# Kernel tuning notes

Measured on AMD Instinct MI355X. Metric: run time of the kernel, lower is better.

Reference implementation:

```python
import jax, jax.numpy as jnp
from jax import lax
import numpy as np

B, N, E, F = 32, 256, 8, 16
NEIGH = 31            # neighbourhood_size
K1 = NEIGH + 1        # subgraph size = neigh_size + 1


def setup_inputs() -> dict:
    rng = np.random.default_rng(0)
    # Connected symmetric adjacency: backbone chain + random extra pairs (no self loops).
    A = np.zeros((B, N, N), np.float32)
    i = np.arange(N - 1)
    A[:, i, i + 1] = 1.0
    A[:, i + 1, i] = 1.0
    for b in range(B):
        pairs = rng.integers(0, N, size=(N, 2))
        pairs = pairs[pairs[:, 0] != pairs[:, 1]]
        A[b, pairs[:, 0], pairs[:, 1]] = 1.0
        A[b, pairs[:, 1], pairs[:, 0]] = 1.0
    A[:, np.arange(N), np.arange(N)] = 0.0
    key = jax.random.key(0)
    k1, k2 = jax.random.split(key)
    edges = jax.random.normal(k1, (B, N, N, E), dtype=jnp.float32)
    feats = jax.random.normal(k2, (B, N, F), dtype=jnp.float32)
    return {"adj_batch": jnp.asarray(A), "edges_batch": edges, "features_batch": feats}


def _bfs(adj_bool, start):
    """Ordered BFS from `start`, collecting K1 vertices (matches get_neighbours:
    FIFO queue, neighbours enqueued in ascending index order, dedup vs seen)."""
    n = adj_bool.shape[0]
    queue = jnp.zeros((n + 1,), jnp.int32).at[0].set(start)  # slot n is a dummy sink
    seen = jnp.zeros((n,), bool).at[start].set(True)
    processed = jnp.zeros((K1,), jnp.int32)

    def body(i, st):
        queue, seen, head, tail, processed = st
        cur = queue[head]
        processed = processed.at[i].set(cur)
        nbr = adj_bool[cur] & ~seen                      # new frontier, index order
        cum = jnp.cumsum(nbr.astype(jnp.int32))
        pos = jnp.where(nbr, tail + cum - 1, n)          # compacted queue slots
        queue = queue.at[pos].set(jnp.arange(n, dtype=jnp.int32))
        return queue, seen | nbr, head + 1, tail + cum[-1], processed

    st = lax.fori_loop(0, K1, body, (queue, seen, jnp.int32(0), jnp.int32(1), processed))
    return st[4]  # [K1] BFS ordering


def reference(adj_batch, edges_batch, features_batch):
    adj_bool = adj_batch != 0
    starts = jnp.arange(adj_batch.shape[1], dtype=jnp.int32)
    # proc: [B, N, K1] local->original vertex mapping per (graph, centre vertex)
    proc = jax.vmap(lambda ab: jax.vmap(lambda s: _bfs(ab, s))(starts))(adj_bool)

    def gather(adj, edges, feats, p):
        pi = p[:, :, None]                               # [N, K1, 1]
        pj = p[:, None, :]                               # [N, 1, K1]
        sub_adj = adj[pi, pj]                            # [N, K1, K1]
        mask = (sub_adj != 0)[..., None]
        sub_edges = jnp.where(mask, edges[pi, pj], 0.0)  # [N, K1, K1, E]
        sub_feats = feats[p]                             # [N, K1, F]
        return sub_adj, sub_edges, sub_feats

    return jax.vmap(gather)(adj_batch, edges_batch, features_batch, proc)
```

## Files before the change

### kernel.cpp

```cpp
#include <hip/hip_runtime.h>
#include <stdint.h>

#define Bb 32
#define Nn 256
#define Ee 8
#define Ff 16
#define K1 32

typedef unsigned long long u64;
typedef float f32x4 __attribute__((ext_vector_type(4)));

__global__ void bitmask_kernel(const float* __restrict__ adj, u64* __restrict__ bm) {
    int wave = (blockIdx.x << 2) + (threadIdx.x >> 6);
    int lane = threadIdx.x & 63;
    const float* row = adj + (size_t)wave * Nn;
#pragma unroll
    for (int w = 0; w < 4; ++w) {
        float v = row[w * 64 + lane];
        u64 m = __ballot(v != 0.0f);
        if (lane == 0) bm[(size_t)wave * 4 + w] = m;
    }
}

__global__ void bfs2_kernel(const u64* __restrict__ bm,
                            uint32_t* __restrict__ proc32,
                            uint32_t* __restrict__ submask_g) {
    __shared__ u64 bml[Nn * 4];
    __shared__ uint8_t order[4][K1];
    __shared__ uint32_t subm[4][K1];
    int blk = blockIdx.x;
    int b = blk >> 6;
    int t = threadIdx.x;
    int wv = t >> 6, l = t & 63;

#pragma unroll
    for (int k = 0; k < 4; ++k) bml[t + k * 256] = bm[(size_t)b * 1024 + t + k * 256];
    __syncthreads();

    int s = ((blk & 63) << 2) + wv;
    u64 seen[4];
#pragma unroll
    for (int q = 0; q < 4; ++q) seen[q] = (q == (s >> 6)) ? (1ull << (s & 63)) : 0ull;
    if (l == 0) order[wv][0] = (uint8_t)s;
    u64 lpre = (1ull << l) - 1ull;
    int count = 1;
    for (int i = 0; i < K1; ++i) {
        int cur = order[wv][i];
#pragma unroll
        for (int q = 0; q < 4; ++q) {
            u64 nw = bml[cur * 4 + q] & ~seen[q];
            seen[q] |= nw;
            int pos = count + __popcll(nw & lpre);
            if (((nw >> l) & 1ull) && pos < K1)
                order[wv][pos] = (uint8_t)((q << 6) + l);
            count += __popcll(nw);
        }
        if (count >= K1) break;
    }

    int half = l >> 5, j2 = l & 31;
#pragma unroll
    for (int step = 0; step < 16; ++step) {
        int row = order[wv][step * 2 + half];
        int pj = order[wv][j2];
        bool bit = (bml[row * 4 + (pj >> 6)] >> (pj & 63)) & 1ull;
        u64 bal = __ballot(bit);
        if (l == 0)  subm[wv][step * 2]     = (uint32_t)bal;
        if (l == 32) subm[wv][step * 2 + 1] = (uint32_t)(bal >> 32);
    }

    const uint32_t* o32 = (const uint32_t*)&order[wv][0];
    if (l < 8) proc32[((size_t)b * 256 + s) * 8 + l] = o32[l];
    if (l < 32) submask_g[((size_t)b * 256 + s) * 32 + l] = subm[wv][l];
}

__global__ void gather_kernel(const f32x4* __restrict__ e4,
                              const f32x4* __restrict__ feats4,
                              const uint32_t* __restrict__ proc32,
                              const uint32_t* __restrict__ submask_g,
                              float* __restrict__ out) {
    int bs = blockIdx.x;
    int b = bs >> 8;
    int t = threadIdx.x;
    __shared__ int p[K1];
    __shared__ uint32_t sm[K1];

    if (t < 8) {
        uint32_t w = proc32[(size_t)bs * 8 + t];
        p[t * 4 + 0] = w & 255;
        p[t * 4 + 1] = (w >> 8) & 255;
        p[t * 4 + 2] = (w >> 16) & 255;
        p[t * 4 + 3] = (w >> 24) & 255;
    }
    if (t >= 64 && t < 96) sm[t - 64] = submask_g[(size_t)bs * 32 + (t - 64)];
    __syncthreads();

    f32x4* out0 = (f32x4*)(out) + (size_t)bs * 256;
    {
        int i = t >> 3;
        int j0 = (t & 7) * 4;
        uint32_t m = sm[i];
        f32x4 a;
        a.x = (float)((m >> (j0 + 0)) & 1u);
        a.y = (float)((m >> (j0 + 1)) & 1u);
        a.z = (float)((m >> (j0 + 2)) & 1u);
        a.w = (float)((m >> (j0 + 3)) & 1u);
        out0[t] = a;
    }

    f32x4* out2 = (f32x4*)(out + 75497472ull) + (size_t)bs * 128;
    if (t < 128) {
        int i = t >> 2, f4 = t & 3;
        out2[t] = feats4[((size_t)b * 256 + p[i]) * 4 + f4];
    }

    f32x4* out1 = (f32x4*)(out + 8388608ull) + (size_t)bs * 2048;
#pragma unroll
    for (int k = 0; k < 8; ++k) {
        int v = t + k * 256;
        int i = v >> 6, j = (v >> 1) & 31, h = v & 1;
        bool m = (sm[i] >> j) & 1u;
        f32x4 val = (f32x4){0.f, 0.f, 0.f, 0.f};
        if (m) val = e4[(((size_t)b * 256 + p[i]) * 256 + p[j]) * 2 + h];
        out1[v] = val;
    }
}

extern "C" void kernel_launch(void* const* d_in, const int* in_sizes, int n_in,
                              void* d_out, int out_size, void* d_ws, size_t ws_size,
                              hipStream_t stream) {
    const float* adj   = (const float*)d_in[0];
    const float* edges = (const float*)d_in[1];
    const float* feats = (const float*)d_in[2];
    float* out = (float*)d_out;

    u64* bm = (u64*)d_ws;
    uint32_t* proc32  = (uint32_t*)((char*)d_ws + (256 << 10));
    uint32_t* submask = (uint32_t*)((char*)d_ws + (512 << 10));

    bitmask_kernel<<<Bb * Nn / 4, 256, 0, stream>>>(adj, bm);
    bfs2_kernel<<<2048, 256, 0, stream>>>(bm, proc32, submask);
    gather_kernel<<<Bb * Nn, 256, 0, stream>>>((const f32x4*)edges, (const f32x4*)feats,
                                               proc32, submask, out);
}
```

Before: 81.80 us.

## Split gather into edge kernel and separate zero/adjacency fill kernel

The single gather kernel becomes two kernels. An edge kernel writes only the pairs of edge entries where at least one adjacency bit is set. A fill kernel writes the sub-adjacency floats and zero-fills the edge pairs whose mask bits are both clear. Each thread now handles two j entries (32 bytes each) so global stores are wider, and the sparse gather work is kept apart from the dense zero writes. The cost is an extra kernel launch, and the two kernels' branchy work splits may leave lanes idle.

```diff
diff --git a/kernel.cpp b/kernel.cpp
--- a/kernel.cpp
+++ b/kernel.cpp
@@ -74,11 +74,49 @@
     if (l < 32) submask_g[((size_t)b * 256 + s) * 32 + l] = subm[wv][l];
 }
 
-__global__ void gather_kernel(const f32x4* __restrict__ e4,
-                              const f32x4* __restrict__ feats4,
-                              const uint32_t* __restrict__ proc32,
-                              const uint32_t* __restrict__ submask_g,
-                              float* __restrict__ out) {
+__global__ void fill_kernel(const uint32_t* __restrict__ submask_g,
+                            float* __restrict__ out) {
+    int bs = blockIdx.x;
+    int t = threadIdx.x;
+    __shared__ uint32_t sm[K1];
+    if (t < 32) sm[t] = submask_g[(size_t)bs * 32 + t];
+    __syncthreads();
+
+    f32x4* out0 = (f32x4*)(out) + (size_t)bs * 256;
+    {
+        int i = t >> 3;
+        int j0 = (t & 7) * 4;
+        uint32_t m = sm[i];
+        f32x4 a;
+        a.x = (float)((m >> (j0 + 0)) & 1u);
+        a.y = (float)((m >> (j0 + 1)) & 1u);
+        a.z = (float)((m >> (j0 + 2)) & 1u);
+        a.w = (float)((m >> (j0 + 3)) & 1u);
+        out0[t] = a;
+    }
+
+    f32x4* out1 = (f32x4*)(out + 8388608ull) + (size_t)bs * 2048;
+    f32x4 z = (f32x4){0.f, 0.f, 0.f, 0.f};
+#pragma unroll
+    for (int k = 0; k < 2; ++k) {
+        int L = t + k * 256;
+        int i = L >> 4, jp = L & 15;
+        uint32_t m2 = (sm[i] >> (jp * 2)) & 3u;
+        if (m2 == 0) {
+            int v0 = L * 4;
+            out1[v0 + 0] = z;
+            out1[v0 + 1] = z;
+            out1[v0 + 2] = z;
+            out1[v0 + 3] = z;
+        }
+    }
+}
+
+__global__ void edge_kernel(const f32x4* __restrict__ e4,
+                            const f32x4* __restrict__ feats4,
+                            const uint32_t* __restrict__ proc32,
+                            const uint32_t* __restrict__ submask_g,
+                            float* __restrict__ out) {
     int bs = blockIdx.x;
     int b = bs >> 8;
     int t = threadIdx.x;
@@ -95,19 +133,6 @@
     if (t >= 64 && t < 96) sm[t - 64] = submask_g[(size_t)bs * 32 + (t - 64)];
     __syncthreads();
 
-    f32x4* out0 = (f32x4*)(out) + (size_t)bs * 256;
-    {
-        int i = t >> 3;
-        int j0 = (t & 7) * 4;
-        uint32_t m = sm[i];
-        f32x4 a;
-        a.x = (float)((m >> (j0 + 0)) & 1u);
-        a.y = (float)((m >> (j0 + 1)) & 1u);
-        a.z = (float)((m >> (j0 + 2)) & 1u);
-        a.w = (float)((m >> (j0 + 3)) & 1u);
-        out0[t] = a;
-    }
-
     f32x4* out2 = (f32x4*)(out + 75497472ull) + (size_t)bs * 128;
     if (t < 128) {
         int i = t >> 2, f4 = t & 3;
@@ -116,13 +141,27 @@
 
     f32x4* out1 = (f32x4*)(out + 8388608ull) + (size_t)bs * 2048;
 #pragma unroll
-    for (int k = 0; k < 8; ++k) {
-        int v = t + k * 256;
-        int i = v >> 6, j = (v >> 1) & 31, h = v & 1;
-        bool m = (sm[i] >> j) & 1u;
-        f32x4 val = (f32x4){0.f, 0.f, 0.f, 0.f};
-        if (m) val = e4[(((size_t)b * 256 + p[i]) * 256 + p[j]) * 2 + h];
-        out1[v] = val;
+    for (int k = 0; k < 2; ++k) {
+        int L = t + k * 256;
+        int i = L >> 4, jp = L & 15;
+        uint32_t m2 = (sm[i] >> (jp * 2)) & 3u;
+        if (m2) {
+            int pi = p[i];
+#pragma unroll
+            for (int d = 0; d < 2; ++d) {
+                int j = jp * 2 + d;
+                f32x4 v0 = (f32x4){0.f, 0.f, 0.f, 0.f};
+                f32x4 v1 = v0;
+                if ((m2 >> d) & 1u) {
+                    int pj = p[j];
+                    size_t eb = (((size_t)b * 256 + pi) * 256 + pj) * 2;
+                    v0 = e4[eb];
+                    v1 = e4[eb + 1];
+                }
+                out1[L * 4 + d * 2 + 0] = v0;
+                out1[L * 4 + d * 2 + 1] = v1;
+            }
+        }
     }
 }
 
@@ -140,6 +179,7 @@
 
     bitmask_kernel<<<Bb * Nn / 4, 256, 0, stream>>>(adj, bm);
     bfs2_kernel<<<2048, 256, 0, stream>>>(bm, proc32, submask);
-    gather_kernel<<<Bb * Nn, 256, 0, stream>>>((const f32x4*)edges, (const f32x4*)feats,
-                                               proc32, submask, out);
+    edge_kernel<<<Bb * Nn, 256, 0, stream>>>((const f32x4*)edges, (const f32x4*)feats,
+                                             proc32, submask, out);
+    fill_kernel<<<Bb * Nn, 256, 0, stream>>>(submask, out);
 }
```

Result: slower. 123.3 us (+50.7%).
